# Kernel tuning notes

Hardware: AMD Instinct MI355X
Metric: run time of the kernel (lower is better)

Reference implementation:

```python
import jax, jax.numpy as jnp
import numpy as np

N, C, EMB, OUT, HID, HEADS, K, R, E = 100000, 256, 256, 8, 256, 4, 20000, 16, 800000
RETR_IN = EMB + OUT + 1  # z_retr + o_retr + retr_score
DH = HID // HEADS


def _lin(key, fi, fo):
    return jax.random.normal(key, (fi, fo), jnp.float32) / np.sqrt(fi)


def setup_inputs() -> dict:
    key = jax.random.key(0)
    ks = jax.random.split(key, 32)
    inp = {
        "h_cone": jax.random.normal(ks[0], (N, C), jnp.float32),
        "z_retr": jax.random.normal(ks[1], (K, R, EMB), jnp.float32),
        "o_retr": jax.random.normal(ks[2], (K, R, OUT), jnp.float32),
        "retr_score": jax.random.uniform(ks[3], (K, R), jnp.float32),
        "teacher_yhat": jax.random.normal(ks[4], (N, OUT), jnp.float32),
        "outpin_nids": jax.random.randint(ks[5], (K,), 0, N, jnp.int32),
        "edge_index": jax.random.randint(ks[6], (2, E), 0, N, jnp.int32),
        # retr_proj: Linear(RETR_IN,HID) -> ReLU -> Linear(HID,HID)
        "rp_W1": _lin(ks[7], RETR_IN, HID), "rp_b1": jnp.zeros((HID,), jnp.float32),
        "rp_W2": _lin(ks[8], HID, HID),     "rp_b2": jnp.zeros((HID,), jnp.float32),
        # query_proj: Linear(C, HID)
        "qp_W": _lin(ks[9], C, HID), "qp_b": jnp.zeros((HID,), jnp.float32),
        # MultiheadAttention packed q/k/v projection + output projection
        "in_proj_W": _lin(ks[10], HID, 3 * HID), "in_proj_b": jnp.zeros((3 * HID,), jnp.float32),
        "out_proj_W": _lin(ks[11], HID, HID),    "out_proj_b": jnp.zeros((HID,), jnp.float32),
        # gate_net: Linear(C+HID,HID) -> ReLU -> Linear(HID,C) -> Sigmoid
        "gate_W1": _lin(ks[12], C + HID, HID), "gate_b1": jnp.zeros((HID,), jnp.float32),
        "gate_W2": _lin(ks[13], HID, C),       "gate_b2": jnp.zeros((C,), jnp.float32),
        # update_net: Linear(HID,C) -> ReLU -> Linear(C,C)
        "upd_W1": _lin(ks[14], HID, C), "upd_b1": jnp.zeros((C,), jnp.float32),
        "upd_W2": _lin(ks[15], C, C),   "upd_b2": jnp.zeros((C,), jnp.float32),
        # cone GNN (LocalGNN gcn, 2 layers): C->HID, HID->HID with sym-normalized aggregation
        "gnn_W1": _lin(ks[16], C, HID),   "gnn_b1": jnp.zeros((HID,), jnp.float32),
        "gnn_W2": _lin(ks[17], HID, HID), "gnn_b2": jnp.zeros((HID,), jnp.float32),
        # head: Linear(HID,HID) -> ReLU -> Linear(HID,OUT) (orig zero-init; random here for nontrivial grads)
        "head_W1": _lin(ks[18], HID, HID), "head_b1": jnp.zeros((HID,), jnp.float32),
        "head_W2": _lin(ks[19], HID, OUT) * 0.01, "head_b2": jnp.zeros((OUT,), jnp.float32),
    }
    return inp


def _forward(h_cone, z_retr, o_retr, retr_score, teacher_yhat, outpin_nids, edge_index,
             rp_W1, rp_b1, rp_W2, rp_b2, qp_W, qp_b, in_proj_W, in_proj_b,
             out_proj_W, out_proj_b, gate_W1, gate_b1, gate_W2, gate_b2,
             upd_W1, upd_b1, upd_W2, upd_b2, gnn_W1, gnn_b1, gnn_W2, gnn_b2,
             head_W1, head_b1, head_W2, head_b2):
    # ---- retrieval aggregation: per-outpin cross-attn over R neighbors ----
    kv_in = jnp.concatenate([z_retr, o_retr, retr_score[..., None]], axis=-1)  # [K,R,RETR_IN]
    kv = jax.nn.relu(kv_in @ rp_W1 + rp_b1) @ rp_W2 + rp_b2                    # [K,R,HID]
    hq = h_cone[outpin_nids]                                                   # [K,C] gather
    q = hq @ qp_W + qp_b                                                       # [K,HID]
    Wq, Wk, Wv = jnp.split(in_proj_W, 3, axis=1)
    bq, bk, bv = jnp.split(in_proj_b, 3)
    qh = (q @ Wq + bq).reshape(K, HEADS, DH)
    kh = (kv @ Wk + bk).reshape(K, R, HEADS, DH)
    vh = (kv @ Wv + bv).reshape(K, R, HEADS, DH)
    att = jax.nn.softmax(jnp.einsum('khd,krhd->khr', qh, kh) / np.sqrt(DH), axis=-1)
    ctx = jnp.einsum('khr,krhd->khd', att, vh).reshape(K, HID)
    retr_ctx = ctx @ out_proj_W + out_proj_b                                   # [K,HID]
    # ---- gated outpin fusion + scatter back ----
    gate = jax.nn.sigmoid(jax.nn.relu(jnp.concatenate([hq, retr_ctx], axis=-1) @ gate_W1 + gate_b1) @ gate_W2 + gate_b2)
    update = jax.nn.relu(retr_ctx @ upd_W1 + upd_b1) @ upd_W2 + upd_b2         # [K,C]
    h = h_cone.at[outpin_nids].set(hq + gate * update)                         # scatter
    # ---- cone GNN: 2-layer GCN with self loops, symmetric normalization ----
    loops = jnp.arange(N, dtype=edge_index.dtype)
    src = jnp.concatenate([edge_index[0], loops])
    dst = jnp.concatenate([edge_index[1], loops])
    deg = jax.ops.segment_sum(jnp.ones_like(src, jnp.float32), dst, num_segments=N)
    norm = (jax.lax.rsqrt(deg[src]) * jax.lax.rsqrt(deg[dst]))[:, None]
    x1 = h @ gnn_W1 + gnn_b1
    h1 = jax.nn.relu(jax.ops.segment_sum(x1[src] * norm, dst, num_segments=N))
    x2 = h1 @ gnn_W2 + gnn_b2
    h2 = jax.ops.segment_sum(x2[src] * norm, dst, num_segments=N)
    # ---- residual head ----
    delta = jax.nn.relu(h2 @ head_W1 + head_b1) @ head_W2 + head_b2
    return teacher_yhat + delta


def reference(h_cone, z_retr, o_retr, retr_score, teacher_yhat, outpin_nids, edge_index,
              rp_W1, rp_b1, rp_W2, rp_b2, qp_W, qp_b, in_proj_W, in_proj_b,
              out_proj_W, out_proj_b, gate_W1, gate_b1, gate_W2, gate_b2,
              upd_W1, upd_b1, upd_W2, upd_b2, gnn_W1, gnn_b1, gnn_W2, gnn_b2,
              head_W1, head_b1, head_W2, head_b2):
    return _forward(h_cone, z_retr, o_retr, retr_score, teacher_yhat, outpin_nids, edge_index,
                    rp_W1, rp_b1, rp_W2, rp_b2, qp_W, qp_b, in_proj_W, in_proj_b,
                    out_proj_W, out_proj_b, gate_W1, gate_b1, gate_W2, gate_b2,
                    upd_W1, upd_b1, upd_W2, upd_b2, gnn_W1, gnn_b1, gnn_W2, gnn_b2,
                    head_W1, head_b1, head_W2, head_b2)
```

## Files before the change

kernel.cpp:

```cpp
#include <hip/hip_runtime.h>
#include <cstdint>
#include <cstddef>

typedef unsigned short u16;

#define NN    100000
#define OUTD  8
#define KKP   20000
#define RR    16
#define EE    800000
#define KRR   (KKP*RR)
#define KP    20096
#define NP    100096

typedef __bf16 v8bf __attribute__((ext_vector_type(8)));
typedef float  v4f  __attribute__((ext_vector_type(4)));

__device__ __forceinline__ float b2f(u16 u) {
    union { uint32_t i; float f; } v; v.i = (uint32_t)u << 16; return v.f;
}
__device__ __forceinline__ u16 f2b(float f) {
    union { float f; uint32_t i; } v; v.f = f;
    uint32_t i = v.i;
    return (u16)((i + 0x7fffu + ((i >> 16) & 1u)) >> 16);
}
__device__ __forceinline__ uint32_t pk2(float a, float b) {
    return (uint32_t)f2b(a) | ((uint32_t)f2b(b) << 16);
}

#define GLDS(g, l) __builtin_amdgcn_global_load_lds(                         \
    (const __attribute__((address_space(1))) void*)(g),                      \
    (__attribute__((address_space(3))) void*)(l), 16, 0, 0)

#define WAITVL(n) asm volatile("s_waitcnt vmcnt(" #n ") lgkmcnt(0)" ::: "memory")
#define BAR() __builtin_amdgcn_s_barrier()

template <int EPI, int OMODE, int A32, int RETR>
__launch_bounds__(256)
__global__ void gemm_bf_k(const void* __restrict__ Av, int lda, int M, int Ka,
                          const u16* __restrict__ Wt,
                          const float* __restrict__ bias,
                          void* __restrict__ Cv, int ldc,
                          const float* __restrict__ o_ex,
                          const float* __restrict__ s_ex,
                          const float* __restrict__ Wex)
{
    constexpr int NBA = A32 ? 2 : 3;
    __shared__ u16 As[NBA * 128 * 32];
    __shared__ u16 Bs[3 * 128 * 32];
    const int row0 = blockIdx.x * 128;
    const int col0 = blockIdx.y * 128;
    const int t    = threadIdx.x;
    const int lane = t & 63;
    const int w    = t >> 6;
    const int wm   = w & 1, wn = w >> 1;

    const int idx0 = t, idx1 = t + 256;
    const u16* Ab = (const u16*)Av;
    const float* Af = (const float*)Av;
    const u16* Ag0 = Ab + (size_t)(row0 + (idx0 >> 2)) * lda + (idx0 & 3) * 8;
    const u16* Ag1 = Ab + (size_t)(row0 + (idx1 >> 2)) * lda + (idx1 & 3) * 8;
    const float* Af0 = Af + (size_t)(row0 + (idx0 >> 2)) * lda + (idx0 & 3) * 8;
    const float* Af1 = Af + (size_t)(row0 + (idx1 >> 2)) * lda + (idx1 & 3) * 8;
    const u16* Bg0 = Wt + (size_t)(col0 + (idx0 >> 2)) * Ka + (idx0 & 3) * 8;
    const u16* Bg1 = Wt + (size_t)(col0 + (idx1 >> 2)) * Ka + (idx1 & 3) * 8;
    const int s0 = idx0 * 8, s1 = idx1 * 8;

    auto stageB = [&](int bi, int kk) {
        u16* bp = Bs + bi * (128 * 32);
        GLDS(Bg0 + kk, bp + s0);
        GLDS(Bg1 + kk, bp + s1);
    };
    auto stageA = [&](int bi, int kk) {
        u16* ap = As + bi * (128 * 32);
        GLDS(Ag0 + kk, ap + s0);
        GLDS(Ag1 + kk, ap + s1);
    };

    float4 P0, P1, P2, P3, Q0, Q1, Q2, Q3;
    auto loadP = [&](int kk) {
        P0 = *(const float4*)(Af0 + kk);     P1 = *(const float4*)(Af0 + kk + 4);
        P2 = *(const float4*)(Af1 + kk);     P3 = *(const float4*)(Af1 + kk + 4);
    };
    auto loadQ = [&](int kk) {
        Q0 = *(const float4*)(Af0 + kk);     Q1 = *(const float4*)(Af0 + kk + 4);
        Q2 = *(const float4*)(Af1 + kk);     Q3 = *(const float4*)(Af1 + kk + 4);
    };
    auto writeP = [&](int bi) {
        u16* ap = As + bi * (128 * 32);
        uint4 u0, u1;
        u0.x = pk2(P0.x, P0.y); u0.y = pk2(P0.z, P0.w);
        u0.z = pk2(P1.x, P1.y); u0.w = pk2(P1.z, P1.w);
        u1.x = pk2(P2.x, P2.y); u1.y = pk2(P2.z, P2.w);
        u1.z = pk2(P3.x, P3.y); u1.w = pk2(P3.z, P3.w);
        *(uint4*)(ap + s0) = u0;
        *(uint4*)(ap + s1) = u1;
    };
    auto writeQ = [&](int bi) {
        u16* ap = As + bi * (128 * 32);
        uint4 u0, u1;
        u0.x = pk2(Q0.x, Q0.y); u0.y = pk2(Q0.z, Q0.w);
        u0.z = pk2(Q1.x, Q1.y); u0.w = pk2(Q1.z, Q1.w);
        u1.x = pk2(Q2.x, Q2.y); u1.y = pk2(Q2.z, Q2.w);
        u1.z = pk2(Q3.x, Q3.y); u1.w = pk2(Q3.z, Q3.w);
        *(uint4*)(ap + s0) = u0;
        *(uint4*)(ap + s1) = u1;
    };

    v4f acc[4][4];
#pragma unroll
    for (int mi = 0; mi < 4; mi++)
#pragma unroll
        for (int ni = 0; ni < 4; ni++) acc[mi][ni] = 0.f;

    const int fr = lane & 15;
    const int fq = (lane >> 4) * 8;
    const int nk = Ka >> 5;

    if (A32) {
        loadP(0);
        stageB(0, 0);
        if (nk > 1) {
            loadQ(32);
            stageB(1, 32);
        }
        writeP(0);
        if (nk > 1) { WAITVL(6); }
        else        { WAITVL(0); }
    } else {
        stageA(0, 0); stageB(0, 0);
        if (nk > 1) { stageA(1, 32); stageB(1, 32); WAITVL(4); }
        else        { WAITVL(0); }
    }
    BAR();

    int rb = 0, sb = 2;
    for (int tI = 0; tI < nk; ++tI) {
        const bool st = (tI + 2) < nk;
        const int kk2 = (tI + 2) << 5;
        if (st) {
            if (A32) {
                if (tI & 1) loadQ(kk2); else loadP(kk2);
                stageB(sb, kk2);
            } else {
                stageA(sb, kk2);
                stageB(sb, kk2);
            }
        }
        const u16* Ar = As + (A32 ? (tI & 1) : rb) * (128 * 32);
        const u16* Br = Bs + rb * (128 * 32);
        v8bf af[4], bv[4];
#pragma unroll
        for (int mi = 0; mi < 4; mi++)
            af[mi] = *(const v8bf*)&Ar[(wm * 64 + mi * 16 + fr) * 32 + fq];
#pragma unroll
        for (int ni = 0; ni < 4; ni++)
            bv[ni] = *(const v8bf*)&Br[(wn * 64 + ni * 16 + fr) * 32 + fq];
#pragma unroll
        for (int mi = 0; mi < 4; mi++)
#pragma unroll
            for (int ni = 0; ni < 4; ni++)
                acc[mi][ni] = __builtin_amdgcn_mfma_f32_16x16x32_bf16(
                    af[mi], bv[ni], acc[mi][ni], 0, 0, 0);

        if (tI + 1 < nk) {
            if (A32) {
                if (tI & 1) writeP((tI + 1) & 1); else writeQ((tI + 1) & 1);
            }
            if (st) { if (A32) { WAITVL(6); } else { WAITVL(4); } }
            else    { WAITVL(0); }
            BAR();
        }
        rb = (rb == 2) ? 0 : rb + 1;
        sb = (sb == 2) ? 0 : sb + 1;
    }

    const int crow = wm * 64 + (lane >> 4) * 4;
    const int ccol = wn * 64 + (lane & 15);
    float bias_v[4];
#pragma unroll
    for (int ni = 0; ni < 4; ni++) bias_v[ni] = bias[col0 + ccol + ni * 16];

    u16*   Cb = (u16*)Cv;
    float* Cf = (float*)Cv;
#pragma unroll
    for (int mi = 0; mi < 4; mi++) {
#pragma unroll
        for (int reg = 0; reg < 4; reg++) {
            int r = row0 + crow + mi * 16 + reg;
            if (r >= M) continue;
            float ov[8], sv;
            if (RETR) {
#pragma unroll
                for (int u = 0; u < 8; u++) ov[u] = o_ex[(size_t)r * 8 + u];
                sv = s_ex[r];
            }
#pragma unroll
            for (int ni = 0; ni < 4; ni++) {
                int c = col0 + ccol + ni * 16;
                float v = acc[mi][ni][reg] + bias_v[ni];
                if (RETR) {
                    float e = sv * Wex[8 * 256 + c];
#pragma unroll
                    for (int u = 0; u < 8; u++) e = fmaf(ov[u], Wex[u * 256 + c], e);
                    v += e;
                }
                if (EPI == 1) v = fmaxf(v, 0.f);
                if (EPI == 2) v = 1.f / (1.f + expf(-v));
                if (OMODE == 1) Cb[(size_t)r * ldc + c] = f2b(v);
                else            Cf[(size_t)r * ldc + c] = v;
            }
        }
    }
}

__launch_bounds__(256, 1)
__global__ void retrfuse_k(const float* __restrict__ Zf,
                           const u16*  __restrict__ W1t,
                           const float* __restrict__ b1,
                           const float* __restrict__ o_ex,
                           const float* __restrict__ s_ex,
                           const u16*  __restrict__ wqk,
                           const u16*  __restrict__ Wv,
                           const float* __restrict__ bv2,
                           u16* __restrict__ ctx)
{
    __shared__ __align__(16) u16 Az[128 * 256];
    __shared__ __align__(16) u16 Ax[128 * 32];
    __shared__ __align__(16) u16 Bp[2 * 128 * 32];
    __shared__ __align__(16) u16 Hs[128 * 256];

    float* attL = (float*)Bp;

    const int bx = blockIdx.x;
    const int row0 = bx * 128;
    const int t = threadIdx.x, lane = t & 63, w = t >> 6;
    const int wm = w & 1, wn = w >> 1;
    const int fr = lane & 15, fq = (lane >> 4) * 8;
    const int idx0 = t, idx1 = t + 256;

    auto stageBt = [&](int tts) {
        int p2 = (tts >= 9) ? 1 : 0;
        int s2 = tts - p2 * 9;
        const u16* g0 = W1t + (size_t)(p2 * 128 + (idx0 >> 2)) * 288 + (idx0 & 3) * 8 + s2 * 32;
        const u16* g1 = W1t + (size_t)(p2 * 128 + (idx1 >> 2)) * 288 + (idx1 & 3) * 8 + s2 * 32;
        u16* bp = Bp + (tts & 1) * (128 * 32);
        GLDS(g0, bp + idx0 * 8);
        GLDS(g1, bp + idx1 * 8);
    };

    {
        const float* zb = Zf + (size_t)row0 * 256;
        float4 pa[4], pb[4];
#pragma unroll
        for (int j = 0; j < 4; j++) {
            int c = j * 256 + t, r = c >> 5, sl = c & 31;
            const float* g = zb + (size_t)r * 256 + sl * 8;
            pa[j] = *(const float4*)g;
            pb[j] = *(const float4*)(g + 4);
        }
        stageBt(0);
#pragma unroll
        for (int j = 0; j < 16; j++) {
            int c = j * 256 + t, r = c >> 5, sl = c & 31;
            int jr = j & 3;
            uint4 u;
            u.x = pk2(pa[jr].x, pa[jr].y); u.y = pk2(pa[jr].z, pa[jr].w);
            u.z = pk2(pb[jr].x, pb[jr].y); u.w = pk2(pb[jr].z, pb[jr].w);
            *(uint4*)((char*)Az + (size_t)r * 512 + ((sl ^ (r & 7)) * 16)) = u;
            int jn = j + 4;
            if (jn < 16) {
                int cn = jn * 256 + t, rn = cn >> 5, sn = cn & 31;
                const float* gn = zb + (size_t)rn * 256 + sn * 8;
                pa[jr] = *(const float4*)gn;
                pb[jr] = *(const float4*)(gn + 4);
            }
        }
#pragma unroll
        for (int j = 0; j < 2; j++) {
            int c = j * 256 + t, r = c >> 2, sl = c & 3;
            int rg = row0 + r;
            uint4 u = make_uint4(0u, 0u, 0u, 0u);
            if (sl == 0) {
                float4 o0 = *(const float4*)(o_ex + (size_t)rg * 8);
                float4 o1 = *(const float4*)(o_ex + (size_t)rg * 8 + 4);
                u.x = pk2(o0.x, o0.y); u.y = pk2(o0.z, o0.w);
                u.z = pk2(o1.x, o1.y); u.w = pk2(o1.z, o1.w);
            } else if (sl == 1) {
                u.x = pk2(s_ex[rg], 0.f);
            }
            *(uint4*)((char*)Ax + r * 64 + ((sl ^ (r & 3)) * 16)) = u;
        }
        WAITVL(0);
        BAR();
    }

    v4f acc[4][4];
#pragma unroll
    for (int mi = 0; mi < 4; mi++)
#pragma unroll
        for (int ni = 0; ni < 4; ni++) acc[mi][ni] = 0.f;

    for (int tt = 0; tt < 18; ++tt) {
        if (tt + 1 < 18) stageBt(tt + 1);
        const int pass = (tt >= 9) ? 1 : 0;
        const int s = tt - pass * 9;
        const u16* Br = Bp + (tt & 1) * (128 * 32);
        v8bf af[4], bb[4];
#pragma unroll
        for (int mi = 0; mi < 4; mi++) {
            int row = wm * 64 + mi * 16 + fr;
            if (s < 8)
                af[mi] = *(const v8bf*)((const char*)Az + (size_t)row * 512 +
                                        (((s * 4 + (fq >> 3)) ^ (row & 7)) * 16));
            else
                af[mi] = *(const v8bf*)((const char*)Ax + row * 64 +
                                        (((fq >> 3) ^ (row & 3)) * 16));
        }
#pragma unroll
        for (int ni = 0; ni < 4; ni++)
            bb[ni] = *(const v8bf*)&Br[(wn * 64 + ni * 16 + fr) * 32 + fq];
#pragma unroll
        for (int mi = 0; mi < 4; mi++)
#pragma unroll
            for (int ni = 0; ni < 4; ni++)
                acc[mi][ni] = __builtin_amdgcn_mfma_f32_16x16x32_bf16(
                    af[mi], bb[ni], acc[mi][ni], 0, 0, 0);

        if (s == 8) {
            const int col0p = pass * 128;
            const int crow = wm * 64 + (lane >> 4) * 4;
            const int ccol = wn * 64 + fr;
            float bvv[4];
#pragma unroll
            for (int ni = 0; ni < 4; ni++) bvv[ni] = b1[col0p + ccol + ni * 16];
#pragma unroll
            for (int mi = 0; mi < 4; mi++)
#pragma unroll
                for (int reg = 0; reg < 4; reg++) {
                    int rl = crow + mi * 16 + reg;
#pragma unroll
                    for (int ni = 0; ni < 4; ni++) {
                        int c = col0p + ccol + ni * 16;
                        float v = fmaxf(acc[mi][ni][reg] + bvv[ni], 0.f);
                        *(u16*)((char*)Hs + (size_t)rl * 512 +
                                (((c >> 3) ^ (rl & 7)) * 16) + (c & 7) * 2) = f2b(v);
                    }
                }
#pragma unroll
            for (int mi = 0; mi < 4; mi++)
#pragma unroll
                for (int ni = 0; ni < 4; ni++) acc[mi][ni] = 0.f;
        }
        if (tt < 17) { WAITVL(0); BAR(); }
    }

    auto stageV = [&](int rr) {
#pragma unroll
        for (int j = 0; j < 4; j++) {
            int c = j * 256 + t;
            int tile = c >> 9, cc = c & 511;
            int vr = cc >> 5, sp = cc & 31;
            int nts = tile * 8 + rr;
            const u16* g = Wv + (size_t)(nts * 16 + vr) * 256 + ((sp ^ (vr & 7)) * 8);
            GLDS(g, (u16*)((char*)Az + 16384 + (tile * 2 + (rr & 1)) * 8192 + cc * 16));
        }
    };
#pragma unroll
    for (int j = 0; j < 4; j++) {
        int c = j * 256 + t;
        GLDS(wqk + (size_t)(bx * 8) * 1024 + c * 8, (u16*)((char*)Az + c * 16));
    }
    stageV(0);
    WAITVL(4);
    BAR();

#pragma unroll
    for (int kk = 0; kk < 2; kk++) {
        int kloc = w * 2 + kk;
        v4f sc; sc = 0.f;
#pragma unroll
        for (int s = 0; s < 8; s++) {
            int row = kloc * 16 + fr;
            v8bf ha = *(const v8bf*)((const char*)Hs + (size_t)row * 512 +
                                     (((s * 4 + (fq >> 3)) ^ (row & 7)) * 16));
            v4f zf; zf = 0.f;
            v8bf bq = __builtin_bit_cast(v8bf, zf);
            if (fr < 4)
                bq = *(const v8bf*)((const char*)Az + kloc * 2048 + fr * 512 + s * 64 + fq * 2);
            sc = __builtin_amdgcn_mfma_f32_16x16x32_bf16(ha, bq, sc, 0, 0, 0);
        }
        float s0 = sc[0] * 0.125f, s1 = sc[1] * 0.125f;
        float s2 = sc[2] * 0.125f, s3 = sc[3] * 0.125f;
        float mx = fmaxf(fmaxf(s0, s1), fmaxf(s2, s3));
        mx = fmaxf(mx, __shfl_xor(mx, 16));
        mx = fmaxf(mx, __shfl_xor(mx, 32));
        float p0 = __expf(s0 - mx), p1 = __expf(s1 - mx);
        float p2 = __expf(s2 - mx), p3 = __expf(s3 - mx);
        float sm = p0 + p1 + p2 + p3;
        sm += __shfl_xor(sm, 16);
        sm += __shfl_xor(sm, 32);
        float inv = 1.f / sm;
        if (fr < 4) {
            float4 a4 = make_float4(p0 * inv, p1 * inv, p2 * inv, p3 * inv);
            *(float4*)&attL[kloc * 64 + fr * 16 + (lane >> 4) * 4] = a4;
        }
    }
    WAITVL(0);
    BAR();

    const int khalf = w & 1, nth = w >> 1;
    v8bf af4[4][8];
#pragma unroll
    for (int kj = 0; kj < 4; kj++) {
        int row = (khalf * 4 + kj) * 16 + fr;
#pragma unroll
        for (int s = 0; s < 8; s++)
            af4[kj][s] = *(const v8bf*)((const char*)Hs + (size_t)row * 512 +
                                        (((s * 4 + (fq >> 3)) ^ (row & 7)) * 16));
    }
    for (int r = 0; r < 8; ++r) {
        if (r < 7) stageV(r + 1);
        int nt = nth * 8 + r;
        const char* cb = (const char*)Az + 16384 + (nth * 2 + (r & 1)) * 8192;
        v8bf bvf[8];
#pragma unroll
        for (int s = 0; s < 8; s++)
            bvf[s] = *(const v8bf*)(cb + fr * 512 + (((s * 4 + (fq >> 3)) ^ (fr & 7)) * 16));
        float bvb = bv2[nt * 16 + fr];
#pragma unroll
        for (int kj = 0; kj < 4; kj++) {
            int kloc = khalf * 4 + kj;
            v4f d; d = 0.f;
#pragma unroll
            for (int s = 0; s < 8; s++)
                d = __builtin_amdgcn_mfma_f32_16x16x32_bf16(af4[kj][s], bvf[s], d, 0, 0, 0);
            float4 av = *(const float4*)&attL[kloc * 64 + (nt >> 2) * 16 + (lane >> 4) * 4];
            float val = av.x * d[0] + av.y * d[1] + av.z * d[2] + av.w * d[3];
            val += __shfl_xor(val, 16);
            val += __shfl_xor(val, 32);
            if (lane < 16)
                ctx[(size_t)(bx * 8 + kloc) * 256 + nt * 16 + lane] = f2b(val + bvb);
        }
        if (r < 7) { WAITVL(4); BAR(); }
    }
}

__global__ void wtpose_k(const float* __restrict__ W, int ld, int coloff,
                         int fi, int Kpad, u16* __restrict__ Wt)
{
    int g = blockIdx.x * 256 + threadIdx.x;
    if (g >= 256 * Kpad) return;
    int o = g / Kpad, i = g - o * Kpad;
    Wt[g] = f2b(i < fi ? W[(size_t)i * ld + coloff + o] : 0.f);
}

__global__ void wfuse_k(const float* __restrict__ A, const float* __restrict__ Binw,
                        int ldb, int off, const float* __restrict__ ba,
                        const float* __restrict__ bb,
                        u16* __restrict__ Wt_out, float* __restrict__ bias_out,
                        float* __restrict__ out32)
{
    __shared__ float As[256];
    __shared__ float bs[256];
    int i = blockIdx.x, j = threadIdx.x;
    As[j] = A[(size_t)i * 256 + j];
    bs[j] = ba[j];
    __syncthreads();
    float acc = 0.f, accb = 0.f;
    for (int m = 0; m < 256; m++) {
        float bv = Binw[(size_t)m * ldb + off + j];
        acc = fmaf(As[m], bv, acc);
        if (i == 0) accb = fmaf(bs[m], bv, accb);
    }
    Wt_out[(size_t)j * 256 + i] = f2b(acc);
    if (out32) out32[(size_t)j * 256 + i] = acc;
    if (i == 0) bias_out[j] = bb[j] + accb;
}

__global__ void qkfuse_k(const float* __restrict__ Qf32, const float* __restrict__ Wk32,
                         const float* __restrict__ bqf,
                         u16* __restrict__ Wtqk, float* __restrict__ bqk)
{
    __shared__ float wk[64];
    __shared__ float bq[64];
    int b = blockIdx.x;
    int h = b >> 8, m = b & 255;
    int c = threadIdx.x;
    if (c < 64) {
        wk[c] = Wk32[(size_t)(h * 64 + c) * 256 + m];
        bq[c] = bqf[h * 64 + c];
    }
    __syncthreads();
    float acc = 0.f;
    for (int d = 0; d < 64; d++)
        acc = fmaf(Qf32[(size_t)(h * 64 + d) * 256 + c], wk[d], acc);
    Wtqk[(size_t)b * 256 + c] = f2b(acc);
    if (c == 0) {
        float ab = 0.f;
        for (int d = 0; d < 64; d++) ab = fmaf(bq[d], wk[d], ab);
        bqk[b] = ab;
    }
}

__global__ void conv_f2b_k(const float* __restrict__ src, u16* __restrict__ dst, size_t n4)
{
    size_t g = (size_t)blockIdx.x * 256 + threadIdx.x;
    if (g >= n4) return;
    float4 v = ((const float4*)src)[g];
    ((ushort4*)dst)[g] = make_ushort4(f2b(v.x), f2b(v.y), f2b(v.z), f2b(v.w));
}

__global__ void gather_hq_k(const float* __restrict__ hc, const int* __restrict__ nids,
                            u16* __restrict__ acat)
{
    int t = threadIdx.x;
    int k = blockIdx.x * 4 + (t >> 6);
    int c = t & 63;
    if (k >= KKP) return;
    int nid = nids[k];
    float4 v = ((const float4*)hc)[(size_t)nid * 64 + c];
    *(ushort4*)&acat[(size_t)k * 512 + c * 4] =
        make_ushort4(f2b(v.x), f2b(v.y), f2b(v.z), f2b(v.w));
}

__global__ void winner_k(const int* __restrict__ nids, int* __restrict__ winner)
{
    int gid = blockIdx.x * 256 + threadIdx.x;
    if (gid < KKP) atomicMax(&winner[nids[gid]], gid);
}

__global__ void scatter_h_k(const int* __restrict__ nids, const int* __restrict__ winner,
                            const float* __restrict__ hc, const float* __restrict__ gate,
                            const float* __restrict__ upd, u16* __restrict__ hb)
{
    int t = threadIdx.x;
    int k = blockIdx.x * 4 + (t >> 6);
    int c = t & 63;
    if (k >= KKP) return;
    int nid = nids[k];
    if (winner[nid] != k) return;
    float4 hv = ((const float4*)hc)[(size_t)nid * 64 + c];
    float4 gv = ((const float4*)gate)[(size_t)k * 64 + c];
    float4 uv = ((const float4*)upd)[(size_t)k * 64 + c];
    *(ushort4*)&hb[(size_t)nid * 256 + c * 4] = make_ushort4(
        f2b(hv.x + gv.x * uv.x), f2b(hv.y + gv.y * uv.y),
        f2b(hv.z + gv.z * uv.z), f2b(hv.w + gv.w * uv.w));
}

__global__ void edge_count_k(const int* __restrict__ dst, int* __restrict__ cnt, int e)
{
    int gid = blockIdx.x * 256 + threadIdx.x;
    if (gid < e) atomicAdd(&cnt[dst[gid]], 1);
}

__global__ void isd_k(const int* __restrict__ cnt, float* __restrict__ isd, int n)
{
    int gid = blockIdx.x * 256 + threadIdx.x;
    if (gid < n) isd[gid] = rsqrtf((float)(cnt[gid] + 1));
}

#define SCANB 1024
__global__ void scan1_k(const int* __restrict__ in, int* __restrict__ out,
                        int* __restrict__ bsums, int n)
{
    __shared__ int s[SCANB];
    int tid = threadIdx.x;
    int gid = blockIdx.x * SCANB + tid;
    int v = (gid < n) ? in[gid] : 0;
    s[tid] = v;
    __syncthreads();
    for (int off = 1; off < SCANB; off <<= 1) {
        int add = (tid >= off) ? s[tid - off] : 0;
        __syncthreads();
        s[tid] += add;
        __syncthreads();
    }
    if (gid < n) out[gid] = s[tid] - v;
    if (tid == SCANB - 1) bsums[blockIdx.x] = s[tid];
}

__global__ void scan2_k(int* bsums, int nb)
{
    if (threadIdx.x == 0 && blockIdx.x == 0) {
        int run = 0;
        for (int i = 0; i < nb; i++) { int v = bsums[i]; bsums[i] = run; run += v; }
    }
}

__global__ void scan3_k(int* __restrict__ out, const int* __restrict__ bsums, int n, int total)
{
    int gid = blockIdx.x * SCANB + threadIdx.x;
    if (gid < n) out[gid] += bsums[blockIdx.x];
    if (gid == 0) out[n] = total;
}

__global__ void csr_scatter_k(const int* __restrict__ src, const int* __restrict__ dst,
                              const int* __restrict__ row_start, int* __restrict__ cursor,
                              const float* __restrict__ isd,
                              int* __restrict__ csr_src, float* __restrict__ csr_w, int e)
{
    int gid = blockIdx.x * 256 + threadIdx.x;
    if (gid < e) {
        int sP = src[gid], dP = dst[gid];
        int pos = row_start[dP] + atomicAdd(&cursor[dP], 1);
        csr_src[pos] = sP;
        csr_w[pos] = isd[sP] * isd[dP];
    }
}

template <int RELU>
__launch_bounds__(256)
__global__ void gnn_agg_k(const u16* __restrict__ x, const int* __restrict__ row_start,
                          const int* __restrict__ csr_src, const float* __restrict__ csr_w,
                          const float* __restrict__ isd, u16* __restrict__ outp)
{
    int node = blockIdx.x * 4 + (threadIdx.x >> 6);
    int lane = threadIdx.x & 63;
    if (node >= NN) return;
    float si = isd[node];
    float sii = si * si;
    ushort4 sv = ((const ushort4*)x)[(size_t)node * 64 + lane];
    float a0 = b2f(sv.x) * sii, a1 = b2f(sv.y) * sii;
    float a2 = b2f(sv.z) * sii, a3 = b2f(sv.w) * sii;
    int s0 = row_start[node], s1 = row_start[node + 1];
    for (int j = s0; j < s1; j++) {
        int sP = csr_src[j];
        float wv = csr_w[j];
        ushort4 v = ((const ushort4*)x)[(size_t)sP * 64 + lane];
        a0 = fmaf(b2f(v.x), wv, a0);
        a1 = fmaf(b2f(v.y), wv, a1);
        a2 = fmaf(b2f(v.z), wv, a2);
        a3 = fmaf(b2f(v.w), wv, a3);
    }
    if (RELU) {
        a0 = fmaxf(a0, 0.f); a1 = fmaxf(a1, 0.f);
        a2 = fmaxf(a2, 0.f); a3 = fmaxf(a3, 0.f);
    }
    ((ushort4*)outp)[(size_t)node * 64 + lane] =
        make_ushort4(f2b(a0), f2b(a1), f2b(a2), f2b(a3));
}

__launch_bounds__(256)
__global__ void head_out_k(const u16* __restrict__ thid, const float* __restrict__ W2,
                           const float* __restrict__ b2, const float* __restrict__ teacher,
                           float* __restrict__ outp, int n)
{
    __shared__ float ts[32][257];
    __shared__ float w2s[256 * 8];
    int t = threadIdx.x;
    int rbase = blockIdx.x * 32;
    for (int i = t; i < 2048; i += 256) w2s[i] = W2[i];
    for (int i = t; i < 32 * 256; i += 256) {
        int rr = i >> 8, cc = i & 255;
        int gr = rbase + rr;
        ts[rr][cc] = (gr < n) ? b2f(thid[(size_t)gr * 256 + cc]) : 0.f;
    }
    __syncthreads();
    int rr = t >> 3, cc = t & 7;
    int gr = rbase + rr;
    if (gr >= n) return;
    float acc = b2[cc];
    for (int kk = 0; kk < 256; kk++)
        acc = fmaf(ts[rr][kk], w2s[kk * 8 + cc], acc);
    outp[(size_t)gr * 8 + cc] = teacher[(size_t)gr * 8 + cc] + acc;
}

extern "C" void kernel_launch(void* const* d_in, const int* in_sizes, int n_in,
                              void* d_out, int out_size, void* d_ws, size_t ws_size,
                              hipStream_t stream)
{
    (void)in_sizes; (void)n_in; (void)out_size; (void)ws_size;
    const float* h_cone     = (const float*)d_in[0];
    const float* z_retr     = (const float*)d_in[1];
    const float* o_retr     = (const float*)d_in[2];
    const float* retr_score = (const float*)d_in[3];
    const float* teacher    = (const float*)d_in[4];
    const int*   nids       = (const int*)d_in[5];
    const int*   edge       = (const int*)d_in[6];
    const float* rp_W1 = (const float*)d_in[7];   const float* rp_b1 = (const float*)d_in[8];
    const float* rp_W2 = (const float*)d_in[9];   const float* rp_b2 = (const float*)d_in[10];
    const float* qp_W  = (const float*)d_in[11];  const float* qp_b  = (const float*)d_in[12];
    const float* inW   = (const float*)d_in[13];  const float* inB   = (const float*)d_in[14];
    const float* outW  = (const float*)d_in[15];  const float* outB  = (const float*)d_in[16];
    const float* gW1   = (const float*)d_in[17];  const float* gB1   = (const float*)d_in[18];
    const float* gW2   = (const float*)d_in[19];  const float* gB2   = (const float*)d_in[20];
    const float* uW1   = (const float*)d_in[21];  const float* uB1   = (const float*)d_in[22];
    const float* uW2   = (const float*)d_in[23];  const float* uB2   = (const float*)d_in[24];
    const float* gnW1  = (const float*)d_in[25];  const float* gnB1  = (const float*)d_in[26];
    const float* gnW2  = (const float*)d_in[27];  const float* gnB2  = (const float*)d_in[28];
    const float* hW1   = (const float*)d_in[29];  const float* hB1   = (const float*)d_in[30];
    const float* hW2   = (const float*)d_in[31];  const float* hB2   = (const float*)d_in[32];
    float* out = (float*)d_out;

    char* ws = (char*)d_ws;
    size_t off = 0;
    auto alloc = [&](size_t bytes) -> void* {
        void* p = ws + off;
        off = (off + bytes + 255) & ~(size_t)255;
        return p;
    };
    u16* hidden = (u16*)alloc((size_t)KRR * 256 * 2);
    u16* ctxb   = (u16*)alloc((size_t)KP * 256 * 2);
    u16* acat   = (u16*)alloc((size_t)KP * 512 * 2);
    u16* ghid   = (u16*)alloc((size_t)KP * 256 * 2);
    float* gate = (float*)alloc((size_t)KP * 256 * 4);
    u16* uhid   = (u16*)alloc((size_t)KP * 256 * 2);
    float* upd  = (float*)alloc((size_t)KP * 256 * 4);
    u16* wqk_g  = (u16*)alloc((size_t)KP * 1024 * 2);
    u16* wt_rp1 = (u16*)alloc(256 * 288 * 2);
    u16* wt_kv  = (u16*)alloc(512 * 256 * 2);
    u16* wt_qf  = (u16*)alloc(256 * 256 * 2);
    u16* wt_o   = (u16*)alloc(256 * 256 * 2);
    u16* wt_g1  = (u16*)alloc(256 * 512 * 2);
    u16* wt_g2  = (u16*)alloc(256 * 256 * 2);
    u16* wt_u1  = (u16*)alloc(256 * 256 * 2);
    u16* wt_u2  = (u16*)alloc(256 * 256 * 2);
    u16* wt_gn1 = (u16*)alloc(256 * 256 * 2);
    u16* wt_gn2 = (u16*)alloc(256 * 256 * 2);
    u16* wt_h1  = (u16*)alloc(256 * 256 * 2);
    u16* wt_qk  = (u16*)alloc(1024 * 256 * 2);
    float* Qf32 = (float*)alloc(256 * 256 * 4);
    float* Wk32 = (float*)alloc(256 * 256 * 4);
    float* bias_kv = (float*)alloc(512 * 4);
    float* bias_qf = (float*)alloc(256 * 4);
    float* bias_qk = (float*)alloc(1024 * 4);
    int*   winner    = (int*)alloc(NN * 4);
    int*   cnt       = (int*)alloc(NN * 4);
    int*   cursor    = (int*)alloc(NN * 4);
    int*   row_start = (int*)alloc((NN + 1) * 4);
    int*   bsums     = (int*)alloc(1024 * 4);
    float* isd       = (float*)alloc(NN * 4);
    int*   csr_src   = (int*)alloc((size_t)EE * 4);
    float* csr_w     = (float*)alloc((size_t)EE * 4);

    const size_t NPE = (size_t)NP * 256;
    u16* gZ0 = hidden;
    u16* gZ1 = hidden + NPE;
    u16* gZ2 = hidden + 2 * NPE;

    const int* esrc = edge;
    const int* edst = edge + EE;

    auto wtp = [&](const float* W, int ld, int coloff, int fi, int Kpad, u16* Wt) {
        wtpose_k<<<(256 * Kpad + 255) / 256, 256, 0, stream>>>(W, ld, coloff, fi, Kpad, Wt);
    };

    hipMemsetAsync(cnt, 0, NN * 4, stream);
    hipMemsetAsync(cursor, 0, NN * 4, stream);
    edge_count_k<<<(EE + 255) / 256, 256, 0, stream>>>(edst, cnt, EE);
    isd_k<<<(NN + 255) / 256, 256, 0, stream>>>(cnt, isd, NN);
    int nb = (NN + SCANB - 1) / SCANB;
    scan1_k<<<nb, SCANB, 0, stream>>>(cnt, row_start, bsums, NN);
    scan2_k<<<1, 64, 0, stream>>>(bsums, nb);
    scan3_k<<<nb, SCANB, 0, stream>>>(row_start, bsums, NN, EE);
    csr_scatter_k<<<(EE + 255) / 256, 256, 0, stream>>>(esrc, edst, row_start, cursor, isd,
                                                        csr_src, csr_w, EE);

    wtp(rp_W1, 256, 0, 265, 288, wt_rp1);
    wfuse_k<<<256, 256, 0, stream>>>(rp_W2, inW, 768, 256, rp_b2, inB + 256,
                                     wt_kv, bias_kv, Wk32);
    wfuse_k<<<256, 256, 0, stream>>>(rp_W2, inW, 768, 512, rp_b2, inB + 512,
                                     wt_kv + 256 * 256, bias_kv + 256, nullptr);
    wfuse_k<<<256, 256, 0, stream>>>(qp_W, inW, 768, 0, qp_b, inB,
                                     wt_qf, bias_qf, Qf32);
    qkfuse_k<<<1024, 256, 0, stream>>>(Qf32, Wk32, bias_qf, wt_qk, bias_qk);
    wtp(outW, 256, 0, 256, 256, wt_o);
    wtp(gW1,  256, 0, 512, 512, wt_g1);
    wtp(gW2,  256, 0, 256, 256, wt_g2);
    wtp(uW1,  256, 0, 256, 256, wt_u1);
    wtp(uW2,  256, 0, 256, 256, wt_u2);
    wtp(gnW1, 256, 0, 256, 256, wt_gn1);
    wtp(gnW2, 256, 0, 256, 256, wt_gn2);
    wtp(hW1,  256, 0, 256, 256, wt_h1);
    gather_hq_k<<<(KKP + 3) / 4, 256, 0, stream>>>(h_cone, nids, acat);

    gemm_bf_k<0, 1, 0, 0><<<dim3((KKP + 127) / 128, 8), 256, 0, stream>>>(
        acat, 512, KKP, 256, wt_qk, bias_qk, wqk_g, 1024, nullptr, nullptr, nullptr);

    retrfuse_k<<<KRR / 128, 256, 0, stream>>>(
        z_retr, wt_rp1, rp_b1, o_retr, retr_score,
        wqk_g, wt_kv + 256 * 256, bias_kv + 256, ctxb);

    gemm_bf_k<0, 1, 0, 0><<<dim3((KKP + 127) / 128, 2), 256, 0, stream>>>(
        ctxb, 256, KKP, 256, wt_o, outB, acat + 256, 512, nullptr, nullptr, nullptr);

    gemm_bf_k<1, 1, 0, 0><<<dim3((KKP + 127) / 128, 2), 256, 0, stream>>>(
        acat, 512, KKP, 512, wt_g1, gB1, ghid, 256, nullptr, nullptr, nullptr);
    gemm_bf_k<2, 2, 0, 0><<<dim3((KKP + 127) / 128, 2), 256, 0, stream>>>(
        ghid, 256, KKP, 256, wt_g2, gB2, gate, 256, nullptr, nullptr, nullptr);
    gemm_bf_k<1, 1, 0, 0><<<dim3((KKP + 127) / 128, 2), 256, 0, stream>>>(
        acat + 256, 512, KKP, 256, wt_u1, uB1, uhid, 256, nullptr, nullptr, nullptr);
    gemm_bf_k<0, 2, 0, 0><<<dim3((KKP + 127) / 128, 2), 256, 0, stream>>>(
        uhid, 256, KKP, 256, wt_u2, uB2, upd, 256, nullptr, nullptr, nullptr);

    conv_f2b_k<<<(int)(((size_t)NN * 64 + 255) / 256), 256, 0, stream>>>(
        h_cone, gZ0, (size_t)NN * 64);
    hipMemsetAsync(winner, 0xFF, NN * 4, stream);
    winner_k<<<(KKP + 255) / 256, 256, 0, stream>>>(nids, winner);
    scatter_h_k<<<(KKP + 3) / 4, 256, 0, stream>>>(nids, winner, h_cone, gate, upd, gZ0);

    gemm_bf_k<0, 1, 0, 0><<<dim3((NN + 127) / 128, 2), 256, 0, stream>>>(
        gZ0, 256, NN, 256, wt_gn1, gnB1, gZ1, 256, nullptr, nullptr, nullptr);
    gnn_agg_k<1><<<(NN + 3) / 4, 256, 0, stream>>>(gZ1, row_start, csr_src, csr_w, isd, gZ2);
    gemm_bf_k<0, 1, 0, 0><<<dim3((NN + 127) / 128, 2), 256, 0, stream>>>(
        gZ2, 256, NN, 256, wt_gn2, gnB2, gZ0, 256, nullptr, nullptr, nullptr);
    gnn_agg_k<0><<<(NN + 3) / 4, 256, 0, stream>>>(gZ0, row_start, csr_src, csr_w, isd, gZ1);
    gemm_bf_k<1, 1, 0, 0><<<dim3((NN + 127) / 128, 2), 256, 0, stream>>>(
        gZ1, 256, NN, 256, wt_h1, hB1, gZ2, 256, nullptr, nullptr, nullptr);
    head_out_k<<<(NN + 31) / 32, 256, 0, stream>>>(gZ2, hW2, hB2, teacher, out, NN);
}
```

Measured before the change: 1.610 ms.

## Restructure retrieval fusion kernel to 512 threads with direct-register weight loads

The fused retrieval kernel moves from 256 to 512 threads per block, so each of eight waves owns a 64-column slab of the first MLP layer and computes all 256 hidden columns in one pass instead of two. W1 fragments are now read straight from global memory into a triple-buffered register ring rather than staged through LDS with a barrier every k-step, which removes most per-step synchronisation. The wqk prefetch is issued at kernel start, and the attention/V stages are re-split so each wave handles one query and half as many V tiles. The cost is a single large LDS allocation (about 152 KB) that limits residency to one block per CU, plus higher register pressure and more global-load latency exposed on the W1 reads.

```diff
diff --git a/kernel.cpp b/kernel.cpp
--- a/kernel.cpp
+++ b/kernel.cpp
@@ -214,7 +214,7 @@
     }
 }
 
-__launch_bounds__(256, 1)
+__launch_bounds__(512, 1)
 __global__ void retrfuse_k(const float* __restrict__ Zf,
                            const u16*  __restrict__ W1t,
                            const float* __restrict__ b1,
@@ -225,60 +225,44 @@
                            const float* __restrict__ bv2,
                            u16* __restrict__ ctx)
 {
-    __shared__ __align__(16) u16 Az[128 * 256];
-    __shared__ __align__(16) u16 Ax[128 * 32];
-    __shared__ __align__(16) u16 Bp[2 * 128 * 32];
-    __shared__ __align__(16) u16 Hs[128 * 256];
-
-    float* attL = (float*)Bp;
+    __shared__ __align__(16) char L[155648];
+    char* AZ = L;
+    char* AX = L + 65536;
+    char* WQ = L + 73728;
+    char* HS = L + 90112;
 
     const int bx = blockIdx.x;
     const int row0 = bx * 128;
     const int t = threadIdx.x, lane = t & 63, w = t >> 6;
     const int wm = w & 1, wn = w >> 1;
     const int fr = lane & 15, fq = (lane >> 4) * 8;
-    const int idx0 = t, idx1 = t + 256;
-
-    auto stageBt = [&](int tts) {
-        int p2 = (tts >= 9) ? 1 : 0;
-        int s2 = tts - p2 * 9;
-        const u16* g0 = W1t + (size_t)(p2 * 128 + (idx0 >> 2)) * 288 + (idx0 & 3) * 8 + s2 * 32;
-        const u16* g1 = W1t + (size_t)(p2 * 128 + (idx1 >> 2)) * 288 + (idx1 & 3) * 8 + s2 * 32;
-        u16* bp = Bp + (tts & 1) * (128 * 32);
-        GLDS(g0, bp + idx0 * 8);
-        GLDS(g1, bp + idx1 * 8);
+
+    auto stageV = [&](int rr) {
+#pragma unroll
+        for (int j = 0; j < 4; j++) {
+            int c = j * 512 + t;
+            int tile = c >> 9, cc = c & 511;
+            int vr = cc >> 5, sp = cc & 31;
+            int nts = tile * 4 + rr;
+            const u16* g = Wv + (size_t)(nts * 16 + vr) * 256 + ((sp ^ (vr & 7)) * 8);
+            GLDS(g, (u16*)(AZ + (tile * 2 + (rr & 1)) * 8192 + cc * 16));
+        }
     };
 
     {
+        GLDS(wqk + (size_t)(bx * 8) * 1024 + t * 8,         (u16*)(WQ + t * 16));
+        GLDS(wqk + (size_t)(bx * 8) * 1024 + (t + 512) * 8, (u16*)(WQ + 8192 + t * 16));
         const float* zb = Zf + (size_t)row0 * 256;
-        float4 pa[4], pb[4];
-#pragma unroll
-        for (int j = 0; j < 4; j++) {
-            int c = j * 256 + t, r = c >> 5, sl = c & 31;
+        float4 pa[8], pb[8];
+#pragma unroll
+        for (int j = 0; j < 8; j++) {
+            int c = j * 512 + t, r = c >> 5, sl = c & 31;
             const float* g = zb + (size_t)r * 256 + sl * 8;
             pa[j] = *(const float4*)g;
             pb[j] = *(const float4*)(g + 4);
         }
-        stageBt(0);
-#pragma unroll
-        for (int j = 0; j < 16; j++) {
-            int c = j * 256 + t, r = c >> 5, sl = c & 31;
-            int jr = j & 3;
-            uint4 u;
-            u.x = pk2(pa[jr].x, pa[jr].y); u.y = pk2(pa[jr].z, pa[jr].w);
-            u.z = pk2(pb[jr].x, pb[jr].y); u.w = pk2(pb[jr].z, pb[jr].w);
-            *(uint4*)((char*)Az + (size_t)r * 512 + ((sl ^ (r & 7)) * 16)) = u;
-            int jn = j + 4;
-            if (jn < 16) {
-                int cn = jn * 256 + t, rn = cn >> 5, sn = cn & 31;
-                const float* gn = zb + (size_t)rn * 256 + sn * 8;
-                pa[jr] = *(const float4*)gn;
-                pb[jr] = *(const float4*)(gn + 4);
-            }
-        }
-#pragma unroll
-        for (int j = 0; j < 2; j++) {
-            int c = j * 256 + t, r = c >> 2, sl = c & 3;
+        {
+            int r = t >> 2, sl = t & 3;
             int rg = row0 + r;
             uint4 u = make_uint4(0u, 0u, 0u, 0u);
             if (sl == 0) {
@@ -289,7 +273,15 @@
             } else if (sl == 1) {
                 u.x = pk2(s_ex[rg], 0.f);
             }
-            *(uint4*)((char*)Ax + r * 64 + ((sl ^ (r & 3)) * 16)) = u;
+            *(uint4*)(AX + r * 64 + ((sl ^ (r & 3)) * 16)) = u;
+        }
+#pragma unroll
+        for (int j = 0; j < 8; j++) {
+            int c = j * 512 + t, r = c >> 5, sl = c & 31;
+            uint4 u;
+            u.x = pk2(pa[j].x, pa[j].y); u.y = pk2(pa[j].z, pa[j].w);
+            u.z = pk2(pb[j].x, pb[j].y); u.w = pk2(pb[j].z, pb[j].w);
+            *(uint4*)(AZ + (size_t)r * 512 + ((sl ^ (r & 7)) * 16)) = u;
         }
         WAITVL(0);
         BAR();
@@ -301,93 +293,76 @@
 #pragma unroll
         for (int ni = 0; ni < 4; ni++) acc[mi][ni] = 0.f;
 
-    for (int tt = 0; tt < 18; ++tt) {
-        if (tt + 1 < 18) stageBt(tt + 1);
-        const int pass = (tt >= 9) ? 1 : 0;
-        const int s = tt - pass * 9;
-        const u16* Br = Bp + (tt & 1) * (128 * 32);
-        v8bf af[4], bb[4];
+    const u16* bp0 = W1t + (size_t)(wn * 64 +  0 + fr) * 288 + fq;
+    const u16* bp1 = W1t + (size_t)(wn * 64 + 16 + fr) * 288 + fq;
+    const u16* bp2 = W1t + (size_t)(wn * 64 + 32 + fr) * 288 + fq;
+    const u16* bp3 = W1t + (size_t)(wn * 64 + 48 + fr) * 288 + fq;
+
+    v8bf bst[3][4];
+#define LDB(st, s) { bst[st][0] = *(const v8bf*)(bp0 + (s) * 32); \
+                     bst[st][1] = *(const v8bf*)(bp1 + (s) * 32); \
+                     bst[st][2] = *(const v8bf*)(bp2 + (s) * 32); \
+                     bst[st][3] = *(const v8bf*)(bp3 + (s) * 32); }
+    LDB(0, 0)
+    LDB(1, 1)
+#pragma unroll
+    for (int s = 0; s < 9; s++) {
+        if (s + 2 < 9) LDB((s + 2) % 3, s + 2)
+        v8bf af[4];
 #pragma unroll
         for (int mi = 0; mi < 4; mi++) {
             int row = wm * 64 + mi * 16 + fr;
             if (s < 8)
-                af[mi] = *(const v8bf*)((const char*)Az + (size_t)row * 512 +
+                af[mi] = *(const v8bf*)(AZ + (size_t)row * 512 +
                                         (((s * 4 + (fq >> 3)) ^ (row & 7)) * 16));
             else
-                af[mi] = *(const v8bf*)((const char*)Ax + row * 64 +
+                af[mi] = *(const v8bf*)(AX + row * 64 +
                                         (((fq >> 3) ^ (row & 3)) * 16));
         }
-#pragma unroll
-        for (int ni = 0; ni < 4; ni++)
-            bb[ni] = *(const v8bf*)&Br[(wn * 64 + ni * 16 + fr) * 32 + fq];
 #pragma unroll
         for (int mi = 0; mi < 4; mi++)
 #pragma unroll
             for (int ni = 0; ni < 4; ni++)
                 acc[mi][ni] = __builtin_amdgcn_mfma_f32_16x16x32_bf16(
-                    af[mi], bb[ni], acc[mi][ni], 0, 0, 0);
-
-        if (s == 8) {
-            const int col0p = pass * 128;
-            const int crow = wm * 64 + (lane >> 4) * 4;
-            const int ccol = wn * 64 + fr;
-            float bvv[4];
-#pragma unroll
-            for (int ni = 0; ni < 4; ni++) bvv[ni] = b1[col0p + ccol + ni * 16];
-#pragma unroll
-            for (int mi = 0; mi < 4; mi++)
-#pragma unroll
-                for (int reg = 0; reg < 4; reg++) {
-                    int rl = crow + mi * 16 + reg;
-#pragma unroll
-                    for (int ni = 0; ni < 4; ni++) {
-                        int c = col0p + ccol + ni * 16;
-                        float v = fmaxf(acc[mi][ni][reg] + bvv[ni], 0.f);
-                        *(u16*)((char*)Hs + (size_t)rl * 512 +
-                                (((c >> 3) ^ (rl & 7)) * 16) + (c & 7) * 2) = f2b(v);
-                    }
+                    af[mi], bst[s % 3][ni], acc[mi][ni], 0, 0, 0);
+    }
+#undef LDB
+
+    {
+        const int crow = wm * 64 + (lane >> 4) * 4;
+        float bvv[4];
+#pragma unroll
+        for (int ni = 0; ni < 4; ni++) bvv[ni] = b1[wn * 64 + fr + ni * 16];
+#pragma unroll
+        for (int mi = 0; mi < 4; mi++)
+#pragma unroll
+            for (int reg = 0; reg < 4; reg++) {
+                int rl = crow + mi * 16 + reg;
+#pragma unroll
+                for (int ni = 0; ni < 4; ni++) {
+                    int c = wn * 64 + ni * 16 + fr;
+                    float v = fmaxf(acc[mi][ni][reg] + bvv[ni], 0.f);
+                    *(u16*)(HS + (size_t)rl * 512 +
+                            (((c >> 3) ^ (rl & 7)) * 16) + (c & 7) * 2) = f2b(v);
                 }
-#pragma unroll
-            for (int mi = 0; mi < 4; mi++)
-#pragma unroll
-                for (int ni = 0; ni < 4; ni++) acc[mi][ni] = 0.f;
-        }
-        if (tt < 17) { WAITVL(0); BAR(); }
-    }
-
-    auto stageV = [&](int rr) {
-#pragma unroll
-        for (int j = 0; j < 4; j++) {
-            int c = j * 256 + t;
-            int tile = c >> 9, cc = c & 511;
-            int vr = cc >> 5, sp = cc & 31;
-            int nts = tile * 8 + rr;
-            const u16* g = Wv + (size_t)(nts * 16 + vr) * 256 + ((sp ^ (vr & 7)) * 8);
-            GLDS(g, (u16*)((char*)Az + 16384 + (tile * 2 + (rr & 1)) * 8192 + cc * 16));
-        }
-    };
-#pragma unroll
-    for (int j = 0; j < 4; j++) {
-        int c = j * 256 + t;
-        GLDS(wqk + (size_t)(bx * 8) * 1024 + c * 8, (u16*)((char*)Az + c * 16));
-    }
-    stageV(0);
-    WAITVL(4);
-    BAR();
-
-#pragma unroll
-    for (int kk = 0; kk < 2; kk++) {
-        int kloc = w * 2 + kk;
+            }
+        WAITVL(0);
+        BAR();
+    }
+
+    {
+        stageV(0);
+        const int kloc = w;
         v4f sc; sc = 0.f;
 #pragma unroll
         for (int s = 0; s < 8; s++) {
             int row = kloc * 16 + fr;
-            v8bf ha = *(const v8bf*)((const char*)Hs + (size_t)row * 512 +
+            v8bf ha = *(const v8bf*)(HS + (size_t)row * 512 +
                                      (((s * 4 + (fq >> 3)) ^ (row & 7)) * 16));
             v4f zf; zf = 0.f;
             v8bf bq = __builtin_bit_cast(v8bf, zf);
             if (fr < 4)
-                bq = *(const v8bf*)((const char*)Az + kloc * 2048 + fr * 512 + s * 64 + fq * 2);
+                bq = *(const v8bf*)(WQ + kloc * 2048 + fr * 512 + s * 64 + fq * 2);
             sc = __builtin_amdgcn_mfma_f32_16x16x32_bf16(ha, bq, sc, 0, 0, 0);
         }
         float s0 = sc[0] * 0.125f, s1 = sc[1] * 0.125f;
@@ -403,46 +378,52 @@
         float inv = 1.f / sm;
         if (fr < 4) {
             float4 a4 = make_float4(p0 * inv, p1 * inv, p2 * inv, p3 * inv);
-            *(float4*)&attL[kloc * 64 + fr * 16 + (lane >> 4) * 4] = a4;
-        }
-    }
-    WAITVL(0);
-    BAR();
-
-    const int khalf = w & 1, nth = w >> 1;
-    v8bf af4[4][8];
-#pragma unroll
-    for (int kj = 0; kj < 4; kj++) {
-        int row = (khalf * 4 + kj) * 16 + fr;
-#pragma unroll
-        for (int s = 0; s < 8; s++)
-            af4[kj][s] = *(const v8bf*)((const char*)Hs + (size_t)row * 512 +
-                                        (((s * 4 + (fq >> 3)) ^ (row & 7)) * 16));
-    }
-    for (int r = 0; r < 8; ++r) {
-        if (r < 7) stageV(r + 1);
-        int nt = nth * 8 + r;
-        const char* cb = (const char*)Az + 16384 + (nth * 2 + (r & 1)) * 8192;
-        v8bf bvf[8];
-#pragma unroll
-        for (int s = 0; s < 8; s++)
-            bvf[s] = *(const v8bf*)(cb + fr * 512 + (((s * 4 + (fq >> 3)) ^ (fr & 7)) * 16));
-        float bvb = bv2[nt * 16 + fr];
+            *(float4*)(WQ + kloc * 2048 + fr * 64 + (lane >> 4) * 16) = a4;
+        }
+        WAITVL(0);
+        BAR();
+    }
+
+    {
+        const int khalf = w & 1, nth = w >> 1;
+        float bvbs[4];
+#pragma unroll
+        for (int r = 0; r < 4; r++) bvbs[r] = bv2[(nth * 4 + r) * 16 + fr];
+        v8bf af4[4][8];
 #pragma unroll
         for (int kj = 0; kj < 4; kj++) {
-            int kloc = khalf * 4 + kj;
-            v4f d; d = 0.f;
+            int row = (khalf * 4 + kj) * 16 + fr;
 #pragma unroll
             for (int s = 0; s < 8; s++)
-                d = __builtin_amdgcn_mfma_f32_16x16x32_bf16(af4[kj][s], bvf[s], d, 0, 0, 0);
-            float4 av = *(const float4*)&attL[kloc * 64 + (nt >> 2) * 16 + (lane >> 4) * 4];
-            float val = av.x * d[0] + av.y * d[1] + av.z * d[2] + av.w * d[3];
-            val += __shfl_xor(val, 16);
-            val += __shfl_xor(val, 32);
-            if (lane < 16)
-                ctx[(size_t)(bx * 8 + kloc) * 256 + nt * 16 + lane] = f2b(val + bvb);
-        }
-        if (r < 7) { WAITVL(4); BAR(); }
+                af4[kj][s] = *(const v8bf*)(HS + (size_t)row * 512 +
+                                            (((s * 4 + (fq >> 3)) ^ (row & 7)) * 16));
+        }
+#pragma unroll
+        for (int r = 0; r < 4; ++r) {
+            if (r < 3) stageV(r + 1);
+            int nt = nth * 4 + r;
+            const char* cb = AZ + (nth * 2 + (r & 1)) * 8192;
+            v8bf bvf[8];
+#pragma unroll
+            for (int s = 0; s < 8; s++)
+                bvf[s] = *(const v8bf*)(cb + fr * 512 +
+                                        (((s * 4 + (fq >> 3)) ^ (fr & 7)) * 16));
+#pragma unroll
+            for (int kj = 0; kj < 4; kj++) {
+                int kloc = khalf * 4 + kj;
+                v4f d; d = 0.f;
+#pragma unroll
+                for (int s = 0; s < 8; s++)
+                    d = __builtin_amdgcn_mfma_f32_16x16x32_bf16(af4[kj][s], bvf[s], d, 0, 0, 0);
+                float4 av = *(const float4*)(WQ + kloc * 2048 + nth * 64 + (lane >> 4) * 16);
+                float val = av.x * d[0] + av.y * d[1] + av.z * d[2] + av.w * d[3];
+                val += __shfl_xor(val, 16);
+                val += __shfl_xor(val, 32);
+                if (lane < 16)
+                    ctx[(size_t)(bx * 8 + kloc) * 256 + nt * 16 + lane] = f2b(val + bvbs[r]);
+            }
+            if (r < 3) { WAITVL(4); BAR(); }
+        }
     }
 }
 
@@ -778,7 +759,7 @@
     gemm_bf_k<0, 1, 0, 0><<<dim3((KKP + 127) / 128, 8), 256, 0, stream>>>(
         acat, 512, KKP, 256, wt_qk, bias_qk, wqk_g, 1024, nullptr, nullptr, nullptr);
 
-    retrfuse_k<<<KRR / 128, 256, 0, stream>>>(
+    retrfuse_k<<<KRR / 128, 512, 0, stream>>>(
         z_retr, wt_rp1, rp_b1, o_retr, retr_score,
         wqk_g, wt_kv + 256 * 256, bias_kv + 256, ctxb);
 
```

New measurement: 1.451 ms. 9.9% less time.
